# Kernel optimization log

Hardware: AMD Instinct MI355X
Metric: run time of the kernel (lower is better)

## Reference

```python
import jax, jax.numpy as jnp
import numpy as np

N_NODES = 10000
N_EDGES = 640000
IN_CH = 128
HID = 128
OUT = 2


def setup_inputs() -> dict:
    key = jax.random.key(0)
    ks = jax.random.split(key, 12)
    s_in = 1.0 / np.sqrt(IN_CH)
    s_2h = 1.0 / np.sqrt(2 * HID)
    s_h = 1.0 / np.sqrt(HID)
    return {
        "x": jax.random.normal(ks[0], (N_NODES, IN_CH), dtype=jnp.float32),
        "edge_index": jax.random.randint(ks[1], (2, N_EDGES), 0, N_NODES, dtype=jnp.int64),
        # SAGEConv: lin_l applied to aggregated neighbors (has bias), lin_r to self (no bias)
        "W_l": jax.random.uniform(ks[2], (IN_CH, HID), jnp.float32, -s_in, s_in),
        "b_l": jax.random.uniform(ks[3], (HID,), jnp.float32, -s_in, s_in),
        "W_r": jax.random.uniform(ks[4], (IN_CH, HID), jnp.float32, -s_in, s_in),
        # lin0: in -> hid
        "W0": jax.random.uniform(ks[5], (IN_CH, HID), jnp.float32, -s_in, s_in),
        "b0": jax.random.uniform(ks[6], (HID,), jnp.float32, -s_in, s_in),
        # lin1: 2*hid -> hid
        "W1": jax.random.uniform(ks[7], (2 * HID, HID), jnp.float32, -s_2h, s_2h),
        "b1": jax.random.uniform(ks[8], (HID,), jnp.float32, -s_2h, s_2h),
        # lin2: hid -> out
        "W2": jax.random.uniform(ks[9], (HID, OUT), jnp.float32, -s_h, s_h),
        "b2": jax.random.uniform(ks[10], (OUT,), jnp.float32, -s_h, s_h),
    }


def reference(x, edge_index, W_l, b_l, W_r, W0, b0, W1, b1, W2, b2):
    src, dst = edge_index[0], edge_index[1]
    # SAGE mean aggregation: gather source features, scatter-mean onto dst nodes
    msgs = x[src]                                                # [E, in]
    agg = jax.ops.segment_sum(msgs, dst, num_segments=N_NODES)  # [N, in]
    deg = jax.ops.segment_sum(jnp.ones((src.shape[0],), x.dtype), dst,
                              num_segments=N_NODES)              # [N]
    agg = agg / jnp.maximum(deg, 1.0)[:, None]
    # SAGEConv output: lin_l(agg) + lin_r(x)
    h = agg @ W_l + b_l + x @ W_r                                # [N, hid]
    h = jax.nn.relu(h)
    h = jnp.max(h, axis=-2)                                      # [hid] global max pool over nodes
    # concat branch: news node is x[0]
    news = jax.nn.relu(x[0] @ W0 + b0)                           # [hid]
    h = jax.nn.relu(jnp.concatenate([news, h], axis=-1) @ W1 + b1)
    return h @ W2 + b2                                           # [out]
```

## Files before the change

kernel.cpp:

```cpp
#include <hip/hip_runtime.h>
#include <hip/hip_bf16.h>

#define NCH 128
#define NPART 256
#define NRANGE 512
#define SEGCAP 24
#define SEGSTR 32
#define RCAP 2560
#define PSMAX 32

typedef __attribute__((ext_vector_type(8))) short bfrag;
typedef __attribute__((ext_vector_type(4))) float ffrag;
typedef __attribute__((ext_vector_type(2))) float f32x2;

__device__ inline unsigned int f2bf_pair(float lo, float hi) {
    unsigned int ul = __float_as_uint(lo);
    unsigned int uh = __float_as_uint(hi);
    ul = (ul + 0x7fffu + ((ul >> 16) & 1u)) >> 16;
    uh = (uh + 0x7fffu + ((uh >> 16) & 1u)) & 0xffff0000u;
    return (ul & 0xffffu) | uh;
}

__device__ inline void gchunk16(const unsigned short* scsr, int base, int i,
                                const unsigned int* __restrict__ xqU, int lq,
                                int half, float& a0, float& a1, float& a2,
                                float& a3) {
    int s[16]; unsigned int u[16];
#pragma unroll
    for (int j = 0; j < 16; ++j) s[j] = scsr[base + i + 2 * j + half];
#pragma unroll
    for (int j = 0; j < 16; ++j) u[j] = xqU[s[j] * 32 + lq];
#pragma unroll
    for (int j = 0; j < 16; ++j) {
        f32x2 v0 = __builtin_amdgcn_cvt_pk_f32_fp8(u[j], false);
        f32x2 v1 = __builtin_amdgcn_cvt_pk_f32_fp8(u[j], true);
        a0 += v0.x; a1 += v0.y; a2 += v1.x; a3 += v1.y;
    }
}

__device__ inline void gtail(const unsigned short* scsr, int base, int i, int d,
                             const unsigned int* __restrict__ xqU, int lq,
                             int half, float& a0, float& a1, float& a2,
                             float& a3) {
    int s[16]; unsigned int u[16];
#pragma unroll
    for (int j = 0; j < 16; ++j) {
        int idx = i + 2 * j + half;
        s[j] = scsr[base + min(idx, d - 1)];
    }
#pragma unroll
    for (int j = 0; j < 16; ++j) u[j] = xqU[s[j] * 32 + lq];
#pragma unroll
    for (int j = 0; j < 16; ++j) {
        int idx = i + 2 * j + half;
        if (idx < d) {
            f32x2 v0 = __builtin_amdgcn_cvt_pk_f32_fp8(u[j], false);
            f32x2 v1 = __builtin_amdgcn_cvt_pk_f32_fp8(u[j], true);
            a0 += v0.x; a1 += v0.y; a2 += v1.x; a3 += v1.y;
        }
    }
}

__global__ __launch_bounds__(512) void k_partprep(
    const float4* __restrict__ x4, const float* __restrict__ Wl,
    const float* __restrict__ Wr, const int* __restrict__ ei32,
    const long long* __restrict__ ei64, unsigned int* __restrict__ M32,
    unsigned int* __restrict__ Wt32, unsigned int* __restrict__ xqU,
    unsigned int* __restrict__ seg, int nq, int N, int E, int PSr,
    unsigned int Mdiv) {
    const int t = threadIdx.x;
    if (blockIdx.x < NPART) {
        __shared__ int sflag;
        __shared__ int cur[NRANGE];
        if (t < 64) {
            int v = ei32[2 * t + 1];
            unsigned long long b = __ballot(v != 0);
            if (t == 0) sflag = (b == 0ULL) ? 1 : 0;
        }
        for (int i = t; i < NRANGE; i += 512) cur[i] = 0;
        __syncthreads();
        const int flag = sflag;
        const int b = blockIdx.x;
        const int ES = (E + NPART - 1) / NPART;
        const int e0 = b * ES, e1 = min(E, e0 + ES);
        for (int bb = e0; bb < e1; bb += 2048) {
            int ebase = bb + t * 4;
            int m = min(4, e1 - ebase);
            if (m <= 0) continue;
            int src4[4], dst4[4];
            if (m == 4) {
                if (flag) {
                    const int4* ps = (const int4*)(ei64 + ebase);
                    const int4* pd = (const int4*)(ei64 + (size_t)E + ebase);
                    int4 q0 = ps[0], q1 = ps[1];
                    int4 r0 = pd[0], r1 = pd[1];
                    src4[0] = q0.x; src4[1] = q0.z; src4[2] = q1.x; src4[3] = q1.z;
                    dst4[0] = r0.x; dst4[1] = r0.z; dst4[2] = r1.x; dst4[3] = r1.z;
                } else {
                    int4 q = *(const int4*)(ei32 + ebase);
                    int4 r0 = *(const int4*)(ei32 + (size_t)E + ebase);
                    src4[0] = q.x; src4[1] = q.y; src4[2] = q.z; src4[3] = q.w;
                    dst4[0] = r0.x; dst4[1] = r0.y; dst4[2] = r0.z; dst4[3] = r0.w;
                }
            } else {
#pragma unroll
                for (int j = 0; j < 4; ++j) {
                    if (j < m) {
                        if (flag) {
                            src4[j] = (int)ei64[ebase + j];
                            dst4[j] = (int)ei64[(size_t)E + ebase + j];
                        } else {
                            src4[j] = ei32[ebase + j];
                            dst4[j] = ei32[(size_t)E + ebase + j];
                        }
                    }
                }
            }
#pragma unroll
            for (int j = 0; j < 4; ++j) {
                if (j < m) {
                    int dstj = dst4[j];
                    int r = Mdiv ? (int)__umulhi((unsigned int)dstj, Mdiv) : dstj;
                    int dl = dstj - r * PSr;
                    int pos = atomicAdd(&cur[r], 1);
                    if (pos < SEGCAP)
                        seg[((size_t)r * NPART + b) * SEGSTR + 1 + pos] =
                            ((unsigned int)dl << 16) | (unsigned int)src4[j];
                }
            }
        }
        __syncthreads();
        for (int i = t; i < NRANGE; i += 512)
            seg[((size_t)i * NPART + b) * SEGSTR] =
                (unsigned int)min(cur[i], SEGCAP);
        return;
    }
    int i = (int)(blockIdx.x - NPART) * 512 + t;
    if (i < nq) {
        float4 v = x4[i];
        int n = i >> 5, cq = i & 31;
        unsigned int p0 = f2bf_pair(v.x, v.y);
        unsigned int p1 = f2bf_pair(v.z, v.w);
        *(uint2*)(M32 + (size_t)n * 128 + 64 + 2 * cq) = make_uint2(p0, p1);
        unsigned int q = __builtin_amdgcn_cvt_pk_fp8_f32(v.x, v.y, 0u, false);
        q = __builtin_amdgcn_cvt_pk_fp8_f32(v.z, v.w, q, true);
        xqU[(size_t)n * 32 + cq] = q;
        return;
    }
    int j = i - nq;
    if (j < 128 * 128) {
        int c = j & 127, kp = j >> 7;
        int k0 = 2 * kp, k1 = 2 * kp + 1;
        float v0 = (k0 < 128) ? Wl[k0 * 128 + c] : Wr[(k0 - 128) * 128 + c];
        float v1 = (k1 < 128) ? Wl[k1 * 128 + c] : Wr[(k1 - 128) * 128 + c];
        Wt32[c * 128 + kp] = f2bf_pair(v0, v1);
    }
}

__global__ __launch_bounds__(512) void k_aggdense(
    const unsigned int* __restrict__ seg, const unsigned int* __restrict__ M32,
    const unsigned short* __restrict__ xq, const short* __restrict__ Wt,
    const float* __restrict__ bl, float* __restrict__ colmax, int N, int PSr) {
    __shared__ unsigned short scsr[RCAP];
    __shared__ unsigned int aggL[PSMAX * 66];
    __shared__ int hist[PSMAX], startp[PSMAX], cur[PSMAX];
    __shared__ float red[8][32];
    const int r = blockIdx.x;
    const int t = threadIdx.x;
    const int wave = t >> 6, lane = t & 63;

    int mycnt = 0;
    uint4 e0 = make_uint4(0, 0, 0, 0), e1 = make_uint4(0, 0, 0, 0),
          e2 = make_uint4(0, 0, 0, 0), e3 = make_uint4(0, 0, 0, 0),
          e4 = make_uint4(0, 0, 0, 0), e5 = make_uint4(0, 0, 0, 0),
          e6 = make_uint4(0, 0, 0, 0);
    if (t < NPART) {
        const uint4* sp = (const uint4*)(seg + ((size_t)r * NPART + t) * SEGSTR);
        e0 = sp[0]; e1 = sp[1]; e2 = sp[2]; e3 = sp[3];
        mycnt = min((int)e0.x, SEGCAP);
        if (mycnt > 15) {
            e4 = sp[4];
            if (mycnt > 19) e5 = sp[5];
            if (mycnt > 23) e6 = sp[6];
        }
    }

    for (int i = t; i < PSMAX * 66; i += 512) aggL[i] = 0;
    if (t < PSMAX) hist[t] = 0;
    __syncthreads();

#define HIST4(ev, kk)                                                          \
    {                                                                          \
        if ((kk) * 4 + 0 >= 1 && (kk) * 4 + 0 <= mycnt)                        \
            atomicAdd(&hist[(ev).x >> 16], 1);                                 \
        if ((kk) * 4 + 1 <= mycnt) atomicAdd(&hist[(ev).y >> 16], 1);          \
        if ((kk) * 4 + 2 <= mycnt) atomicAdd(&hist[(ev).z >> 16], 1);          \
        if ((kk) * 4 + 3 <= mycnt) atomicAdd(&hist[(ev).w >> 16], 1);          \
    }
    HIST4(e0, 0) HIST4(e1, 1) HIST4(e2, 2) HIST4(e3, 3)
    HIST4(e4, 4) HIST4(e5, 5) HIST4(e6, 6)
#undef HIST4
    __syncthreads();
    if (t < PSMAX) {
        int h = hist[t];
        int ip = h;
#pragma unroll
        for (int off = 1; off < PSMAX; off <<= 1) {
            int u = __shfl_up(ip, off);
            if (lane >= off) ip += u;
        }
        startp[t] = ip - h;
        cur[t] = ip - h;
    }
    __syncthreads();
#define SCAT4(ev, kk)                                                          \
    {                                                                          \
        if ((kk) * 4 + 0 >= 1 && (kk) * 4 + 0 <= mycnt) {                      \
            int p_ = atomicAdd(&cur[(ev).x >> 16], 1);                         \
            if (p_ < RCAP) scsr[p_] = (unsigned short)((ev).x & 0xffffu);      \
        }                                                                      \
        if ((kk) * 4 + 1 <= mycnt) {                                           \
            int p_ = atomicAdd(&cur[(ev).y >> 16], 1);                         \
            if (p_ < RCAP) scsr[p_] = (unsigned short)((ev).y & 0xffffu);      \
        }                                                                      \
        if ((kk) * 4 + 2 <= mycnt) {                                           \
            int p_ = atomicAdd(&cur[(ev).z >> 16], 1);                         \
            if (p_ < RCAP) scsr[p_] = (unsigned short)((ev).z & 0xffffu);      \
        }                                                                      \
        if ((kk) * 4 + 3 <= mycnt) {                                           \
            int p_ = atomicAdd(&cur[(ev).w >> 16], 1);                         \
            if (p_ < RCAP) scsr[p_] = (unsigned short)((ev).w & 0xffffu);      \
        }                                                                      \
    }
    SCAT4(e0, 0) SCAT4(e1, 1) SCAT4(e2, 2) SCAT4(e3, 3)
    SCAT4(e4, 4) SCAT4(e5, 5) SCAT4(e6, 6)
#undef SCAT4
    __syncthreads();

    const int l16 = lane & 15, quad = lane >> 4;
    const int rt = wave & 1, cg = wave >> 1;
    const int lrow = rt * 16 + l16;
    bfrag a[8];
    {
        int mc = min(r * PSr + lrow, N - 1);
#pragma unroll
        for (int kk = 0; kk < 4; ++kk)
            a[4 + kk] = *(const bfrag*)((const short*)(M32 + (size_t)mc * 128 + 64)
                                        + kk * 32 + quad * 8);
    }

    const unsigned int* __restrict__ xqU = (const unsigned int*)xq;
    const int half = lane >> 5, lq = lane & 31;
    for (int li = wave; li < PSr; li += 8) {
        int node = r * PSr + li;
        if (node >= N) break;
        int base = startp[li], d = hist[li];
        float a0 = 0.f, a1 = 0.f, a2 = 0.f, a3 = 0.f;
        int i = 0;
        for (; i + 32 <= d; i += 32)
            gchunk16(scsr, base, i, xqU, lq, half, a0, a1, a2, a3);
        if (i < d)
            gtail(scsr, base, i, d, xqU, lq, half, a0, a1, a2, a3);
        a0 += __shfl_xor(a0, 32);
        a1 += __shfl_xor(a1, 32);
        a2 += __shfl_xor(a2, 32);
        a3 += __shfl_xor(a3, 32);
        float sca = 1.0f / fmaxf((float)d, 1.0f);
        if (half == 0) {
            aggL[li * 66 + 2 * lq]     = f2bf_pair(a0 * sca, a1 * sca);
            aggL[li * 66 + 2 * lq + 1] = f2bf_pair(a2 * sca, a3 * sca);
        }
    }
    __syncthreads();

#pragma unroll
    for (int kk = 0; kk < 4; ++kk)
        a[kk] = *(const bfrag*)((const short*)(aggL + lrow * 66 + kk * 16 + quad * 4));
    float mx[2];
#pragma unroll
    for (int ct = 0; ct < 2; ++ct) {
        int col = cg * 32 + ct * 16 + l16;
        float bv = bl[col];
        ffrag acc = {bv, bv, bv, bv};
        const short* wp = Wt + (size_t)col * 256 + quad * 8;
#pragma unroll
        for (int kk = 0; kk < 8; ++kk) {
            bfrag b = *(const bfrag*)(wp + kk * 32);
            acc = __builtin_amdgcn_mfma_f32_16x16x32_bf16(a[kk], b, acc, 0, 0, 0);
        }
        float lm = 0.f;
#pragma unroll
        for (int rr = 0; rr < 4; ++rr) {
            int lr = rt * 16 + quad * 4 + rr;
            int nd = r * PSr + lr;
            if (lr < PSr && nd < N) lm = fmaxf(lm, fmaxf(acc[rr], 0.f));
        }
        lm = fmaxf(lm, __shfl_xor(lm, 16));
        lm = fmaxf(lm, __shfl_xor(lm, 32));
        mx[ct] = lm;
    }
    if (lane < 16) {
        red[wave][l16]      = mx[0];
        red[wave][16 + l16] = mx[1];
    }
    __syncthreads();
    if (t < 128) {
        int cg2 = t >> 5, wi = t & 31;
        colmax[r * 128 + t] = fmaxf(red[2 * cg2][wi], red[2 * cg2 + 1][wi]);
    }
}

__global__ __launch_bounds__(512) void k_head(
    const float* __restrict__ colmax, const float* __restrict__ x,
    const float* __restrict__ W0, const float* __restrict__ b0,
    const float* __restrict__ W1, const float* __restrict__ b1,
    const float* __restrict__ W2, const float* __restrict__ b2,
    float* __restrict__ out) {
    __shared__ float hs[1280];
    float* cat  = hs;
    float* part = hs + 256;
    float* h1p  = hs + 768;
    float* pr   = hs + 896;
    float* xsp  = hs + 1152;
    const int t = threadIdx.x;
    const int c = t & 127, sg = t >> 7;
    {
        float m = 0.f;
        const float* p = colmax + sg * 128 + c;
#pragma unroll 8
        for (int rr = 0; rr < NRANGE / 4; ++rr) m = fmaxf(m, p[rr * 512]);
        part[sg * 128 + c] = m;
    }
    __syncthreads();
    if (t < 128) {
        xsp[t] = x[t];
        cat[128 + t] = fmaxf(fmaxf(part[t], part[128 + t]),
                             fmaxf(part[256 + t], part[384 + t]));
    }
    __syncthreads();
    {
        float a0 = 0.f, a1 = 0.f, a2 = 0.f, a3 = 0.f;
        int k0 = sg * 32;
#pragma unroll
        for (int j = 0; j < 32; j += 4) {
            a0 += xsp[k0 + j + 0] * W0[(k0 + j + 0) * NCH + c];
            a1 += xsp[k0 + j + 1] * W0[(k0 + j + 1) * NCH + c];
            a2 += xsp[k0 + j + 2] * W0[(k0 + j + 2) * NCH + c];
            a3 += xsp[k0 + j + 3] * W0[(k0 + j + 3) * NCH + c];
        }
        part[sg * 128 + c] = (a0 + a1) + (a2 + a3);
    }
    __syncthreads();
    if (t < 128)
        cat[t] = fmaxf(b0[t] + part[t] + part[128 + t] + part[256 + t] + part[384 + t], 0.f);
    __syncthreads();
    {
        float a0 = 0.f, a1 = 0.f, a2 = 0.f, a3 = 0.f;
        int k0 = sg * 64;
#pragma unroll
        for (int j = 0; j < 64; j += 4) {
            a0 += cat[k0 + j + 0] * W1[(k0 + j + 0) * NCH + c];
            a1 += cat[k0 + j + 1] * W1[(k0 + j + 1) * NCH + c];
            a2 += cat[k0 + j + 2] * W1[(k0 + j + 2) * NCH + c];
            a3 += cat[k0 + j + 3] * W1[(k0 + j + 3) * NCH + c];
        }
        part[sg * 128 + c] = (a0 + a1) + (a2 + a3);
    }
    __syncthreads();
    if (t < 128)
        h1p[t] = fmaxf(b1[t] + part[t] + part[128 + t] + part[256 + t] + part[384 + t], 0.f);
    __syncthreads();
    if (t < 128) {
        float2 w = ((const float2*)W2)[t];
        pr[t]       = h1p[t] * w.x;
        pr[128 + t] = h1p[t] * w.y;
    }
    __syncthreads();
    for (int off = 64; off >= 1; off >>= 1) {
        if (t < off) { pr[t] += pr[t + off]; pr[128 + t] += pr[128 + t + off]; }
        __syncthreads();
    }
    if (t == 0) out[0] = pr[0] + b2[0];
    if (t == 1) out[1] = pr[128] + b2[1];
}

__global__ void k_detect(const int* __restrict__ ei, int* __restrict__ flag) {
    int v = ei[2 * threadIdx.x + 1];
    unsigned long long b = __ballot(v != 0);
    if (threadIdx.x == 0) *flag = (b == 0ULL) ? 1 : 0;
}
__global__ void k_hist(const int* __restrict__ ei32, const long long* __restrict__ ei64,
                       const int* __restrict__ flag, int* __restrict__ cnt, int E) {
    int e = blockIdx.x * blockDim.x + threadIdx.x;
    if (e >= E) return;
    int dst = (*flag) ? (int)ei64[(size_t)E + e] : ei32[(size_t)E + e];
    atomicAdd(&cnt[dst], 1);
}
__global__ void k_scan(const int* __restrict__ cnt, int* __restrict__ row_start, int N) {
    __shared__ int lds[1024];
    int t = threadIdx.x;
    int chunk = (N + 1023) / 1024;
    int base = t * chunk;
    int sum = 0;
    for (int i = 0; i < chunk; ++i) {
        int idx = base + i;
        if (idx < N) sum += cnt[idx];
    }
    lds[t] = sum;
    __syncthreads();
    for (int off = 1; off < 1024; off <<= 1) {
        int v = (t >= off) ? lds[t - off] : 0;
        __syncthreads();
        lds[t] += v;
        __syncthreads();
    }
    int run = (t == 0) ? 0 : lds[t - 1];
    for (int i = 0; i < chunk; ++i) {
        int idx = base + i;
        if (idx < N) { row_start[idx] = run; run += cnt[idx]; }
    }
    if (t == 1023) row_start[N] = run;
}
__global__ void k_fill(const int* __restrict__ ei32, const long long* __restrict__ ei64,
                       const int* __restrict__ flag, const int* __restrict__ row_start,
                       int* __restrict__ cursor, int* __restrict__ csr, int E) {
    int e = blockIdx.x * blockDim.x + threadIdx.x;
    if (e >= E) return;
    int src, dst;
    if (*flag) { src = (int)ei64[e]; dst = (int)ei64[(size_t)E + e]; }
    else       { src = ei32[e];      dst = ei32[(size_t)E + e]; }
    int pos = atomicAdd(&cursor[dst], 1);
    csr[row_start[dst] + pos] = src;
}
__global__ __launch_bounds__(256) void k_agg_linmax(
    const float* __restrict__ x, const int* __restrict__ row_start,
    const int* __restrict__ csr, const float* __restrict__ Wl,
    const float* __restrict__ bl, const float* __restrict__ Wr,
    unsigned int* __restrict__ hmaxU, int N, int E) {
    const int lane = threadIdx.x & 63;
    const int wave = threadIdx.x >> 6;
    const int group = blockIdx.x * 4 + wave;
    const int ngroups = (N + 3) / 4;
    const float2* __restrict__ x2  = (const float2*)x;
    const float2* __restrict__ Wl2 = (const float2*)Wl;
    const float2* __restrict__ Wr2 = (const float2*)Wr;
    const float2* __restrict__ bl2 = (const float2*)bl;
    float2 m = make_float2(0.f, 0.f);
    if (group < ngroups) {
        int n0 = group * 4;
        int s[4], d[4];
#pragma unroll
        for (int q = 0; q < 4; ++q) {
            int n = n0 + q;
            if (n < N) { s[q] = row_start[n]; d[q] = row_start[n + 1] - s[q]; }
            else       { s[q] = 0; d[q] = 0; }
        }
        int maxd = max(max(d[0], d[1]), max(d[2], d[3]));
        float2 acc[4];
#pragma unroll
        for (int q = 0; q < 4; ++q) acc[q] = make_float2(0.f, 0.f);
        int idxv[4] = {0, 0, 0, 0};
        for (int i = 0; i < maxd; ++i) {
            int t = i & 63;
            if (t == 0) {
#pragma unroll
                for (int q = 0; q < 4; ++q) {
                    if (i < d[q]) {
                        int a = s[q] + i + lane;
                        a = (a < E) ? a : (E - 1);
                        idxv[q] = csr[a];
                    }
                }
            }
#pragma unroll
            for (int q = 0; q < 4; ++q) {
                if (i < d[q]) {
                    int src = __shfl(idxv[q], t);
                    float2 v = x2[src * 64 + lane];
                    acc[q].x += v.x; acc[q].y += v.y;
                }
            }
        }
        float2 xv[4];
#pragma unroll
        for (int q = 0; q < 4; ++q) {
            float sc = 1.0f / fmaxf((float)d[q], 1.0f);
            acc[q].x *= sc; acc[q].y *= sc;
            int n = n0 + q;
            xv[q] = (n < N) ? x2[n * 64 + lane] : make_float2(0.f, 0.f);
        }
        float2 o[4];
#pragma unroll
        for (int q = 0; q < 4; ++q) o[q] = bl2[lane];
        for (int j = 0; j < 64; ++j) {
            float2 wl0 = Wl2[(2 * j) * 64 + lane];
            float2 wl1 = Wl2[(2 * j + 1) * 64 + lane];
            float2 wr0 = Wr2[(2 * j) * 64 + lane];
            float2 wr1 = Wr2[(2 * j + 1) * 64 + lane];
#pragma unroll
            for (int q = 0; q < 4; ++q) {
                float ax = __shfl(acc[q].x, j);
                float ay = __shfl(acc[q].y, j);
                float xx = __shfl(xv[q].x, j);
                float xy = __shfl(xv[q].y, j);
                o[q].x += ax * wl0.x + ay * wl1.x + xx * wr0.x + xy * wr1.x;
                o[q].y += ax * wl0.y + ay * wl1.y + xx * wr0.y + xy * wr1.y;
            }
        }
#pragma unroll
        for (int q = 0; q < 4; ++q) {
            if (n0 + q < N) {
                m.x = fmaxf(m.x, fmaxf(o[q].x, 0.f));
                m.y = fmaxf(m.y, fmaxf(o[q].y, 0.f));
            }
        }
    }
    __shared__ float2 red2[4][64];
    red2[wave][lane] = m;
    __syncthreads();
    if (wave == 0) {
#pragma unroll
        for (int ww = 1; ww < 4; ++ww) {
            m.x = fmaxf(m.x, red2[ww][lane].x);
            m.y = fmaxf(m.y, red2[ww][lane].y);
        }
        atomicMax(&hmaxU[2 * lane],     __float_as_uint(m.x));
        atomicMax(&hmaxU[2 * lane + 1], __float_as_uint(m.y));
    }
}
__global__ void k_head_fb(const float* __restrict__ x, const float* __restrict__ hmax,
                          const float* __restrict__ W0, const float* __restrict__ b0,
                          const float* __restrict__ W1, const float* __restrict__ b1,
                          const float* __restrict__ W2, const float* __restrict__ b2,
                          float* __restrict__ out) {
    __shared__ float s_cat[2 * NCH];
    __shared__ float s_part[256];
    __shared__ float s_h1[NCH];
    int t = threadIdx.x;
    if (t < NCH) {
        float acc = b0[t];
        for (int k = 0; k < NCH; ++k) acc += x[k] * W0[k * NCH + t];
        s_cat[t] = fmaxf(acc, 0.f);
        s_cat[NCH + t] = hmax[t];
    }
    __syncthreads();
    {
        int c = t & 127, half = t >> 7;
        float p = 0.f;
        int k0 = half * NCH;
        for (int k = k0; k < k0 + NCH; ++k) p += s_cat[k] * W1[k * NCH + c];
        s_part[t] = p;
    }
    __syncthreads();
    if (t < NCH) s_h1[t] = fmaxf(s_part[t] + s_part[NCH + t] + b1[t], 0.f);
    __syncthreads();
    if (t < 2) {
        float o = b2[t];
        for (int k = 0; k < NCH; ++k) o += s_h1[k] * W2[k * 2 + t];
        out[t] = o;
    }
}

extern "C" void kernel_launch(void* const* d_in, const int* in_sizes, int n_in,
                              void* d_out, int out_size, void* d_ws, size_t ws_size,
                              hipStream_t stream) {
    const float* x  = (const float*)d_in[0];
    const void*  ei = d_in[1];
    const float* Wl = (const float*)d_in[2];
    const float* bl = (const float*)d_in[3];
    const float* Wr = (const float*)d_in[4];
    const float* W0 = (const float*)d_in[5];
    const float* b0 = (const float*)d_in[6];
    const float* W1 = (const float*)d_in[7];
    const float* b1 = (const float*)d_in[8];
    const float* W2 = (const float*)d_in[9];
    const float* b2 = (const float*)d_in[10];
    float* out = (float*)d_out;

    const int N = in_sizes[0] / NCH;
    const int E = in_sizes[1] / 2;
    const int nq = N * 32;
    const int PSr = (N + NRANGE - 1) / NRANGE;

    int* iws = (int*)d_ws;
    float* colmax = (float*)iws;
    unsigned int* seg = (unsigned int*)(iws + NRANGE * 128);
    unsigned int* Wt32 = seg + (size_t)NPART * NRANGE * SEGSTR;
    unsigned int* M32  = Wt32 + 128 * 128;
    unsigned short* xq = (unsigned short*)(M32 + (size_t)N * 128);
    size_t need = ((size_t)NRANGE * 128 + (size_t)NPART * NRANGE * SEGSTR +
                   128 * 128 + (size_t)N * 128 + (size_t)N * 32) * 4;
    bool main_ok = (need <= ws_size) && (N <= NRANGE * PSMAX) && (N <= 65535) &&
                   (PSr >= 1) && (PSr <= PSMAX);

    if (main_ok) {
        unsigned int Mdiv = (PSr > 1)
            ? (unsigned int)(0x100000000ULL / (unsigned long long)PSr + 1ULL)
            : 0u;
        int prepb = (nq + 128 * 128 + 511) / 512;
        k_partprep<<<NPART + prepb, 512, 0, stream>>>(
            (const float4*)x, Wl, Wr, (const int*)ei, (const long long*)ei,
            M32, Wt32, (unsigned int*)xq, seg, nq, N, E, PSr, Mdiv);
        k_aggdense<<<NRANGE, 512, 0, stream>>>(seg, M32, xq,
                                               (const short*)Wt32,
                                               bl, colmax, N, PSr);
        k_head<<<1, 512, 0, stream>>>(colmax, x, W0, b0, W1, b1, W2, b2, out);
        return;
    }

    int* fcnt      = iws;
    int* fcursor   = iws + N;
    unsigned int* fhmax = (unsigned int*)(iws + 2 * N);
    int* flag      = iws + 2 * N + 128;
    int* frs       = iws + 2 * N + 132;
    int* fcsr      = iws + 3 * N + 144;

    hipMemsetAsync(d_ws, 0, (size_t)(2 * N + 128) * sizeof(int), stream);
    k_detect<<<1, 64, 0, stream>>>((const int*)ei, flag);
    k_hist<<<(E + 255) / 256, 256, 0, stream>>>((const int*)ei, (const long long*)ei,
                                                flag, fcnt, E);
    k_scan<<<1, 1024, 0, stream>>>(fcnt, frs, N);
    k_fill<<<(E + 255) / 256, 256, 0, stream>>>((const int*)ei, (const long long*)ei,
                                                flag, frs, fcursor, fcsr, E);
    int ngroups = (N + 3) / 4;
    k_agg_linmax<<<(ngroups + 3) / 4, 256, 0, stream>>>(x, frs, fcsr, Wl, bl, Wr,
                                                        fhmax, N, E);
    k_head_fb<<<1, 256, 0, stream>>>(x, (const float*)fhmax, W0, b0, W1, b1, W2, b2, out);
}
```

Before: 133.2 us.

## Replace fixed-capacity edge segments with compact LDS-sorted per-partition edge lists

```diff
diff --git a/kernel.cpp b/kernel.cpp
--- a/kernel.cpp
+++ b/kernel.cpp
@@ -2,10 +2,9 @@
 #include <hip/hip_bf16.h>
 
 #define NCH 128
-#define NPART 256
+#define NPART 128
+#define ESMAX 5120
 #define NRANGE 512
-#define SEGCAP 24
-#define SEGSTR 32
 #define RCAP 2560
 #define PSMAX 32
 
@@ -66,23 +65,75 @@
     const float* __restrict__ Wr, const int* __restrict__ ei32,
     const long long* __restrict__ ei64, unsigned int* __restrict__ M32,
     unsigned int* __restrict__ Wt32, unsigned int* __restrict__ xqU,
-    unsigned int* __restrict__ seg, int nq, int N, int E, int PSr,
-    unsigned int Mdiv) {
+    unsigned int* __restrict__ edges, unsigned int* __restrict__ cntoff,
+    int nq, int N, int E, int ES, int PSr, unsigned int Mdiv) {
     const int t = threadIdx.x;
     if (blockIdx.x < NPART) {
         __shared__ int sflag;
-        __shared__ int cur[NRANGE];
+        __shared__ int hist[NRANGE], cur[NRANGE];
+        __shared__ unsigned int lbuf[ESMAX];
+        __shared__ int wtot[8];
         if (t < 64) {
             int v = ei32[2 * t + 1];
             unsigned long long b = __ballot(v != 0);
             if (t == 0) sflag = (b == 0ULL) ? 1 : 0;
         }
-        for (int i = t; i < NRANGE; i += 512) cur[i] = 0;
+        hist[t] = 0;
         __syncthreads();
         const int flag = sflag;
         const int b = blockIdx.x;
-        const int ES = (E + NPART - 1) / NPART;
         const int e0 = b * ES, e1 = min(E, e0 + ES);
+        for (int bb = e0; bb < e1; bb += 2048) {
+            int ebase = bb + t * 4;
+            int m = min(4, e1 - ebase);
+            if (m <= 0) continue;
+            int dst4[4];
+            if (m == 4) {
+                if (flag) {
+                    const int4* pd = (const int4*)(ei64 + (size_t)E + ebase);
+                    int4 r0 = pd[0], r1 = pd[1];
+                    dst4[0] = r0.x; dst4[1] = r0.z; dst4[2] = r1.x; dst4[3] = r1.z;
+                } else {
+                    int4 r0 = *(const int4*)(ei32 + (size_t)E + ebase);
+                    dst4[0] = r0.x; dst4[1] = r0.y; dst4[2] = r0.z; dst4[3] = r0.w;
+                }
+            } else {
+#pragma unroll
+                for (int j = 0; j < 4; ++j)
+                    if (j < m)
+                        dst4[j] = flag ? (int)ei64[(size_t)E + ebase + j]
+                                       : ei32[(size_t)E + ebase + j];
+            }
+#pragma unroll
+            for (int j = 0; j < 4; ++j) {
+                if (j < m) {
+                    int dstj = dst4[j];
+                    int r = Mdiv ? (int)__umulhi((unsigned int)dstj, Mdiv) : dstj;
+                    atomicAdd(&hist[r], 1);
+                }
+            }
+        }
+        __syncthreads();
+        {
+            int h = hist[t];
+            int ip = h;
+            const int lane = t & 63, wv = t >> 6;
+#pragma unroll
+            for (int off = 1; off < 64; off <<= 1) {
+                int u = __shfl_up(ip, off);
+                if (lane >= off) ip += u;
+            }
+            if (lane == 63) wtot[wv] = ip;
+            __syncthreads();
+            int wadd = 0;
+#pragma unroll
+            for (int w = 0; w < 8; ++w) wadd += (w < wv) ? wtot[w] : 0;
+            int excl = ip + wadd - h;
+            cntoff[t * NPART + b] =
+                ((unsigned int)excl << 8) | (unsigned int)min(h, 255);
+            cur[t] = excl;
+        }
+        __syncthreads();
         for (int bb = e0; bb < e1; bb += 2048) {
             int ebase = bb + t * 4;
             int m = min(4, e1 - ebase);
@@ -123,16 +174,14 @@
                     int r = Mdiv ? (int)__umulhi((unsigned int)dstj, Mdiv) : dstj;
                     int dl = dstj - r * PSr;
                     int pos = atomicAdd(&cur[r], 1);
-                    if (pos < SEGCAP)
-                        seg[((size_t)r * NPART + b) * SEGSTR + 1 + pos] =
-                            ((unsigned int)dl << 16) | (unsigned int)src4[j];
+                    lbuf[pos] = ((unsigned int)dl << 16) | (unsigned int)src4[j];
                 }
             }
         }
         __syncthreads();
-        for (int i = t; i < NRANGE; i += 512)
-            seg[((size_t)i * NPART + b) * SEGSTR] =
-                (unsigned int)min(cur[i], SEGCAP);
+        const int cnt = e1 - e0;
+        for (int i = t; i < cnt; i += 512)
+            edges[(size_t)b * ES + i] = lbuf[i];
         return;
     }
     int i = (int)(blockIdx.x - NPART) * 512 + t;
@@ -158,48 +207,30 @@
 }
 
 __global__ __launch_bounds__(512) void k_aggdense(
-    const unsigned int* __restrict__ seg, const unsigned int* __restrict__ M32,
-    const unsigned short* __restrict__ xq, const short* __restrict__ Wt,
-    const float* __restrict__ bl, float* __restrict__ colmax, int N, int PSr) {
+    const unsigned int* __restrict__ edges, const unsigned int* __restrict__ cntoff,
+    const unsigned int* __restrict__ M32, const unsigned short* __restrict__ xq,
+    const short* __restrict__ Wt, const float* __restrict__ bl,
+    float* __restrict__ colmax, int N, int ES, int PSr) {
     __shared__ unsigned short scsr[RCAP];
     __shared__ unsigned int aggL[PSMAX * 66];
+    __shared__ unsigned int soff[NPART];
     __shared__ int hist[PSMAX], startp[PSMAX], cur[PSMAX];
     __shared__ float red[8][32];
     const int r = blockIdx.x;
     const int t = threadIdx.x;
     const int wave = t >> 6, lane = t & 63;
 
-    int mycnt = 0;
-    uint4 e0 = make_uint4(0, 0, 0, 0), e1 = make_uint4(0, 0, 0, 0),
-          e2 = make_uint4(0, 0, 0, 0), e3 = make_uint4(0, 0, 0, 0),
-          e4 = make_uint4(0, 0, 0, 0), e5 = make_uint4(0, 0, 0, 0),
-          e6 = make_uint4(0, 0, 0, 0);
-    if (t < NPART) {
-        const uint4* sp = (const uint4*)(seg + ((size_t)r * NPART + t) * SEGSTR);
-        e0 = sp[0]; e1 = sp[1]; e2 = sp[2]; e3 = sp[3];
-        mycnt = min((int)e0.x, SEGCAP);
-        if (mycnt > 15) {
-            e4 = sp[4];
-            if (mycnt > 19) e5 = sp[5];
-            if (mycnt > 23) e6 = sp[6];
-        }
-    }
-
+    if (t < NPART) soff[t] = cntoff[r * NPART + t];
     for (int i = t; i < PSMAX * 66; i += 512) aggL[i] = 0;
     if (t < PSMAX) hist[t] = 0;
     __syncthreads();
 
-#define HIST4(ev, kk)                                                          \
-    {                                                                          \
-        if ((kk) * 4 + 0 >= 1 && (kk) * 4 + 0 <= mycnt)                        \
-            atomicAdd(&hist[(ev).x >> 16], 1);                                 \
-        if ((kk) * 4 + 1 <= mycnt) atomicAdd(&hist[(ev).y >> 16], 1);          \
-        if ((kk) * 4 + 2 <= mycnt) atomicAdd(&hist[(ev).z >> 16], 1);          \
-        if ((kk) * 4 + 3 <= mycnt) atomicAdd(&hist[(ev).w >> 16], 1);          \
-    }
-    HIST4(e0, 0) HIST4(e1, 1) HIST4(e2, 2) HIST4(e3, 3)
-    HIST4(e4, 4) HIST4(e5, 5) HIST4(e6, 6)
-#undef HIST4
+    const int g = t >> 2, sub = t & 3;
+    const unsigned int so = soff[g];
+    const int scnt = (int)(so & 0xffu);
+    const unsigned int* ep = edges + (size_t)g * ES + (so >> 8);
+    for (int k = sub; k < scnt; k += 4)
+        atomicAdd(&hist[ep[k] >> 16], 1);
     __syncthreads();
     if (t < PSMAX) {
         int h = hist[t];
@@ -213,28 +244,11 @@
         cur[t] = ip - h;
     }
     __syncthreads();
-#define SCAT4(ev, kk)                                                          \
-    {                                                                          \
-        if ((kk) * 4 + 0 >= 1 && (kk) * 4 + 0 <= mycnt) {                      \
-            int p_ = atomicAdd(&cur[(ev).x >> 16], 1);                         \
-            if (p_ < RCAP) scsr[p_] = (unsigned short)((ev).x & 0xffffu);      \
-        }                                                                      \
-        if ((kk) * 4 + 1 <= mycnt) {                                           \
-            int p_ = atomicAdd(&cur[(ev).y >> 16], 1);                         \
-            if (p_ < RCAP) scsr[p_] = (unsigned short)((ev).y & 0xffffu);      \
-        }                                                                      \
-        if ((kk) * 4 + 2 <= mycnt) {                                           \
-            int p_ = atomicAdd(&cur[(ev).z >> 16], 1);                         \
-            if (p_ < RCAP) scsr[p_] = (unsigned short)((ev).z & 0xffffu);      \
-        }                                                                      \
-        if ((kk) * 4 + 3 <= mycnt) {                                           \
-            int p_ = atomicAdd(&cur[(ev).w >> 16], 1);                         \
-            if (p_ < RCAP) scsr[p_] = (unsigned short)((ev).w & 0xffffu);      \
-        }                                                                      \
-    }
-    SCAT4(e0, 0) SCAT4(e1, 1) SCAT4(e2, 2) SCAT4(e3, 3)
-    SCAT4(e4, 4) SCAT4(e5, 5) SCAT4(e6, 6)
-#undef SCAT4
+    for (int k = sub; k < scnt; k += 4) {
+        unsigned int e = ep[k];
+        int pos = atomicAdd(&cur[e >> 16], 1);
+        if (pos < RCAP) scsr[pos] = (unsigned short)(e & 0xffffu);
+    }
     __syncthreads();
 
     const int l16 = lane & 15, quad = lane >> 4;
@@ -581,17 +595,20 @@
     const int E = in_sizes[1] / 2;
     const int nq = N * 32;
     const int PSr = (N + NRANGE - 1) / NRANGE;
+    const int ES = (E + NPART - 1) / NPART;
 
     int* iws = (int*)d_ws;
     float* colmax = (float*)iws;
-    unsigned int* seg = (unsigned int*)(iws + NRANGE * 128);
-    unsigned int* Wt32 = seg + (size_t)NPART * NRANGE * SEGSTR;
+    unsigned int* cntoff = (unsigned int*)(iws + NRANGE * 128);
+    unsigned int* edges = cntoff + (size_t)NRANGE * NPART;
+    unsigned int* Wt32 = edges + (size_t)NPART * ESMAX;
     unsigned int* M32  = Wt32 + 128 * 128;
     unsigned short* xq = (unsigned short*)(M32 + (size_t)N * 128);
-    size_t need = ((size_t)NRANGE * 128 + (size_t)NPART * NRANGE * SEGSTR +
-                   128 * 128 + (size_t)N * 128 + (size_t)N * 32) * 4;
+    size_t need = ((size_t)NRANGE * 128 + (size_t)NRANGE * NPART +
+                   (size_t)NPART * ESMAX + 128 * 128 +
+                   (size_t)N * 128 + (size_t)N * 32) * 4;
     bool main_ok = (need <= ws_size) && (N <= NRANGE * PSMAX) && (N <= 65535) &&
-                   (PSr >= 1) && (PSr <= PSMAX);
+                   (PSr >= 1) && (PSr <= PSMAX) && (ES <= ESMAX);
 
     if (main_ok) {
         unsigned int Mdiv = (PSr > 1)
@@ -600,10 +617,10 @@
         int prepb = (nq + 128 * 128 + 511) / 512;
         k_partprep<<<NPART + prepb, 512, 0, stream>>>(
             (const float4*)x, Wl, Wr, (const int*)ei, (const long long*)ei,
-            M32, Wt32, (unsigned int*)xq, seg, nq, N, E, PSr, Mdiv);
-        k_aggdense<<<NRANGE, 512, 0, stream>>>(seg, M32, xq,
+            M32, Wt32, (unsigned int*)xq, edges, cntoff, nq, N, E, ES, PSr, Mdiv);
+        k_aggdense<<<NRANGE, 512, 0, stream>>>(edges, cntoff, M32, xq,
                                                (const short*)Wt32,
-                                               bl, colmax, N, PSr);
+                                               bl, colmax, N, ES, PSr);
         k_head<<<1, 512, 0, stream>>>(colmax, x, W0, b0, W1, b1, W2, b2, out);
         return;
     }
```

Measured after the change: 134.7 us. No clear change (+1.1%).
